# Kernel optimization log

Measured on AMD Instinct MI355X. Metric: run time of the kernel, lower is better.

## Reference

```python
import jax, jax.numpy as jnp
import numpy as np

N_NODES = 100000
N_EDGES = 3200000
IN_DIM = 256
OUT_DIM = 128


def setup_inputs() -> dict:
    key = jax.random.key(0)
    k1, k2, k3, k4, k5 = jax.random.split(key, 5)
    # node features
    x = jax.random.normal(k1, (N_NODES, IN_DIM), dtype=jnp.float32)
    # glorot-uniform weight as in glorot_init
    init_range = np.sqrt(6.0 / (IN_DIM + OUT_DIM)).astype(np.float32)
    weight = jax.random.uniform(k2, (IN_DIM, OUT_DIM), dtype=jnp.float32,
                                minval=-init_range, maxval=init_range)
    # sparse adjacency in COO form: adj[dst, src] = edge_weight
    edge_src = jax.random.randint(k3, (N_EDGES,), 0, N_NODES, dtype=jnp.int64)
    edge_dst = jax.random.randint(k4, (N_EDGES,), 0, N_NODES, dtype=jnp.int64)
    edge_weight = jax.random.uniform(k5, (N_EDGES,), dtype=jnp.float32)
    return {"x": x, "weight": weight, "edge_weight": edge_weight,
            "edge_src": edge_src, "edge_dst": edge_dst}


def reference(x, weight, edge_weight, edge_src, edge_dst):
    # dense feature transform: [N, in] @ [in, out] -> [N, out]
    xw = x @ weight
    # sparse adjacency matmul (adj @ xw) as gather + weighted scatter-add
    msgs = xw[edge_src] * edge_weight[:, None]           # [E, out]
    agg = jax.ops.segment_sum(msgs, edge_dst, num_segments=N_NODES)
    # fused activation
    return jax.nn.relu(agg)
```

## Files before the change

### kernel.cpp

```cpp
#include <hip/hip_runtime.h>

#define IN_DIM 256
#define OUT_DIM 128
#define BM 64
#define BKG 64

#define BSHIFT 7
#define BNODES 128
#define MAXB2 1024
#define CHUNK1 4096
#define CAPB 4736

typedef __attribute__((ext_vector_type(4))) float floatx4;
typedef __attribute__((ext_vector_type(8))) short shortx8;

static __device__ __forceinline__ unsigned short f2bf(float f) {
  unsigned u = __float_as_uint(f);
  u += 0x7FFFu + ((u >> 16) & 1u);
  return (unsigned short)(u >> 16);
}

struct GemmSmem {
  unsigned short As[BM][BKG + 8];
  unsigned short Bs[OUT_DIM][BKG + 8];
};
struct PartSmem {
  uint2 srec[CHUNK1];
  int hcnt[MAXB2];
  int loff[MAXB2];
  int lcur[MAXB2];
  int gbase[MAXB2];
  int sh[256];
};
#define SMEM3 ((sizeof(GemmSmem) > sizeof(PartSmem)) ? sizeof(GemmSmem) : sizeof(PartSmem))

__global__ __launch_bounds__(256) void prep_wt_kernel(
    const float* __restrict__ w, unsigned short* __restrict__ wt) {
  const int idx = blockIdx.x * 256 + threadIdx.x;
  const int k = idx >> 7;
  const int n = idx & 127;
  wt[n * IN_DIM + k] = f2bf(w[idx]);
}

static __device__ void do_gemm_block(int bid, const float* __restrict__ x,
                                     const unsigned short* __restrict__ wt,
                                     unsigned short* __restrict__ xw,
                                     int n_nodes, char* smem) {
  GemmSmem* sm = (GemmSmem*)smem;
  const int t = threadIdx.x;
  const int wv = t >> 6;
  const int lane = t & 63;
  const int quad = lane >> 4;
  const int l16 = lane & 15;
  const int row0 = bid * BM;
  if (row0 >= n_nodes) return;

  floatx4 acc[4][2];
#pragma unroll
  for (int a = 0; a < 4; ++a)
#pragma unroll
    for (int b = 0; b < 2; ++b) acc[a][b] = (floatx4){0.f, 0.f, 0.f, 0.f};

  for (int k0 = 0; k0 < IN_DIM; k0 += BKG) {
    __syncthreads();
#pragma unroll
    for (int i = 0; i < 4; ++i) {
      const int idx = i * 256 + t;
      const int r = idx >> 4;
      const int kq = (idx & 15) * 4;
      int row = row0 + r;
      if (row >= n_nodes) row = n_nodes - 1;
      const float4 v = *(const float4*)(x + (size_t)row * IN_DIM + k0 + kq);
      ushort4 sv;
      sv.x = f2bf(v.x); sv.y = f2bf(v.y); sv.z = f2bf(v.z); sv.w = f2bf(v.w);
      *(ushort4*)&sm->As[r][kq] = sv;
    }
#pragma unroll
    for (int i = 0; i < 4; ++i) {
      const int idx16 = i * 256 + t;
      const int n = idx16 >> 3;
      const int off = (idx16 & 7) * 8;
      *(int4*)&sm->Bs[n][off] =
          *(const int4*)(wt + (size_t)n * IN_DIM + k0 + off);
    }
    __syncthreads();

#pragma unroll
    for (int kk = 0; kk < BKG; kk += 32) {
      shortx8 af[4];
#pragma unroll
      for (int tm = 0; tm < 4; ++tm)
        af[tm] = *(const shortx8*)&sm->As[tm * 16 + l16][kk + quad * 8];
      shortx8 bfr[2];
#pragma unroll
      for (int tn = 0; tn < 2; ++tn)
        bfr[tn] =
            *(const shortx8*)&sm->Bs[wv * 32 + tn * 16 + l16][kk + quad * 8];
#pragma unroll
      for (int tm = 0; tm < 4; ++tm)
#pragma unroll
        for (int tn = 0; tn < 2; ++tn)
          acc[tm][tn] = __builtin_amdgcn_mfma_f32_16x16x32_bf16(
              af[tm], bfr[tn], acc[tm][tn], 0, 0, 0);
    }
  }

#pragma unroll
  for (int tm = 0; tm < 4; ++tm)
#pragma unroll
    for (int tn = 0; tn < 2; ++tn)
#pragma unroll
      for (int r = 0; r < 4; ++r) {
        const int grow = row0 + tm * 16 + quad * 4 + r;
        const int gcol = wv * 32 + tn * 16 + l16;
        if (grow < n_nodes)
          xw[(size_t)grow * OUT_DIM + gcol] = f2bf(acc[tm][tn][r]);
      }
}

static __device__ void do_partition_block(
    int bid, const int* __restrict__ esrc, const int* __restrict__ edst,
    const float* __restrict__ ew, int* __restrict__ btail,
    uint2* __restrict__ csr2, int n_edges, int nb2, char* smem) {
  PartSmem* sm = (PartSmem*)smem;
  const int t = threadIdx.x;
  const int base = bid * CHUNK1;
  const int cn = min(CHUNK1, n_edges - base);

  for (int b = t; b < MAXB2; b += 256) sm->hcnt[b] = 0;
  __syncthreads();

  int dst[16];
  unsigned xpk[16];
#pragma unroll
  for (int i = 0; i < 16; ++i) {
    const int idx = t + i * 256;
    if (idx < cn) {
      const int e = base + idx;
      dst[i] = edst[e];
      unsigned wb = __float_as_uint(ew[e]);
      wb += 0x7FFFu + ((wb >> 16) & 1u);
      xpk[i] = ((wb >> 16) << 17) | (unsigned)esrc[e];
      atomicAdd(&sm->hcnt[((unsigned)dst[i]) >> BSHIFT], 1);
    } else {
      dst[i] = -1;
    }
  }
  __syncthreads();
  {
    const int b4 = 4 * t;
    const int a0 = sm->hcnt[b4], a1 = sm->hcnt[b4 + 1];
    const int a2 = sm->hcnt[b4 + 2], a3 = sm->hcnt[b4 + 3];
    const int s = a0 + a1 + a2 + a3;
    sm->sh[t] = s;
    __syncthreads();
    for (int off = 1; off < 256; off <<= 1) {
      const int add = (t >= off) ? sm->sh[t - off] : 0;
      __syncthreads();
      sm->sh[t] += add;
      __syncthreads();
    }
    int run = sm->sh[t] - s;
    sm->loff[b4] = run; sm->lcur[b4] = run; run += a0;
    sm->loff[b4 + 1] = run; sm->lcur[b4 + 1] = run; run += a1;
    sm->loff[b4 + 2] = run; sm->lcur[b4 + 2] = run; run += a2;
    sm->loff[b4 + 3] = run; sm->lcur[b4 + 3] = run;
  }
  __syncthreads();
  for (int b = t; b < nb2; b += 256) {
    const int c = sm->hcnt[b];
    if (c) sm->gbase[b] = b * CAPB + atomicAdd(&btail[b], c);
  }
  __syncthreads();
#pragma unroll
  for (int i = 0; i < 16; ++i)
    if (dst[i] >= 0) {
      const int bk = ((unsigned)dst[i]) >> BSHIFT;
      const int p = atomicAdd(&sm->lcur[bk], 1);
      sm->srec[p] = make_uint2(xpk[i], (unsigned)dst[i]);
    }
  __syncthreads();
  for (int i = t; i < cn; i += 256) {
    const uint2 r = sm->srec[i];
    const int bk = r.y >> BSHIFT;
    const size_t pos = (size_t)sm->gbase[bk] + (i - sm->loff[bk]);
    if (pos < (size_t)(bk + 1) * CAPB) csr2[pos] = r;
  }
}

__global__ __launch_bounds__(256) void fused_part_gemm_kernel(
    const int* __restrict__ esrc, const int* __restrict__ edst,
    const float* __restrict__ ew, int* __restrict__ btail,
    uint2* __restrict__ csr2, int n_edges, int nb2, int pb,
    const float* __restrict__ x, const unsigned short* __restrict__ wt,
    unsigned short* __restrict__ xw, int n_nodes) {
  __shared__ __align__(16) char smem[SMEM3];
  if ((int)blockIdx.x < pb)
    do_partition_block(blockIdx.x, esrc, edst, ew, btail, csr2, n_edges, nb2,
                       smem);
  else
    do_gemm_block(blockIdx.x - pb, x, wt, xw, n_nodes, smem);
}

struct AggSmem {
  unsigned xin[CAPB];
  unsigned xs[CAPB];
  unsigned char db[CAPB];
  int ncnt[BNODES];
  int lcur[BNODES];
  int sst[BNODES];
  int sen[BNODES];
  int sh[256];
};

__global__ __launch_bounds__(256) void sort_agg_kernel(
    const uint2* __restrict__ csr2, const int* __restrict__ btail,
    const unsigned short* __restrict__ xw, float* __restrict__ out,
    int n_nodes) {
  __shared__ __align__(16) AggSmem sm;
  const int t = threadIdx.x;
  const int b = blockIdx.x;
  const int node0 = b << BSHIFT;
  const size_t S = (size_t)b * CAPB;
  const int cnt = min(btail[b], CAPB);

  for (int i = t; i < cnt; i += 256) {
    const uint2 r = csr2[S + i];
    sm.xin[i] = r.x;
    sm.db[i] = (unsigned char)(r.y & (BNODES - 1));
  }
  if (t < BNODES) sm.ncnt[t] = 0;
  __syncthreads();
  for (int i = t; i < cnt; i += 256) atomicAdd(&sm.ncnt[sm.db[i]], 1);
  __syncthreads();
  {
    const int s = (t < BNODES) ? sm.ncnt[t] : 0;
    sm.sh[t] = s;
    __syncthreads();
    for (int off = 1; off < 256; off <<= 1) {
      const int add = (t >= off) ? sm.sh[t - off] : 0;
      __syncthreads();
      sm.sh[t] += add;
      __syncthreads();
    }
    if (t < BNODES) {
      const int run = sm.sh[t] - s;
      sm.lcur[t] = run;
      sm.sst[t] = run;
      sm.sen[t] = run + s;
    }
  }
  __syncthreads();
  for (int i = t; i < cnt; i += 256) {
    const int p = atomicAdd(&sm.lcur[sm.db[i]], 1);
    sm.xs[p] = sm.xin[i];
  }
  __syncthreads();

  const int g = t >> 4;
  const int lane = t & 15;
  const int d8 = lane * 8;

  for (int nl = g; nl < BNODES; nl += 16) {
    const int node = node0 + nl;
    if (node >= n_nodes) continue;
    const int j0 = sm.sst[nl];
    const int j1 = sm.sen[nl];

    float a0 = 0.f, a1 = 0.f, a2 = 0.f, a3 = 0.f;
    float a4 = 0.f, a5 = 0.f, a6 = 0.f, a7 = 0.f;
    float c0 = 0.f, c1 = 0.f, c2 = 0.f, c3 = 0.f;
    float c4 = 0.f, c5 = 0.f, c6 = 0.f, c7 = 0.f;

    int j = j0;
    for (; j + 4 <= j1; j += 4) {
      const unsigned p0 = sm.xs[j];
      const unsigned p1 = sm.xs[j + 1];
      const unsigned p2 = sm.xs[j + 2];
      const unsigned p3 = sm.xs[j + 3];
      const uint4 v0 = *(const uint4*)(xw + (size_t)(p0 & 0x1FFFFu) * OUT_DIM + d8);
      const uint4 v1 = *(const uint4*)(xw + (size_t)(p1 & 0x1FFFFu) * OUT_DIM + d8);
      const uint4 v2 = *(const uint4*)(xw + (size_t)(p2 & 0x1FFFFu) * OUT_DIM + d8);
      const uint4 v3 = *(const uint4*)(xw + (size_t)(p3 & 0x1FFFFu) * OUT_DIM + d8);
      const float w0 = __uint_as_float((p0 >> 17) << 16);
      const float w1 = __uint_as_float((p1 >> 17) << 16);
      const float w2 = __uint_as_float((p2 >> 17) << 16);
      const float w3 = __uint_as_float((p3 >> 17) << 16);
      a0 = fmaf(__uint_as_float(v0.x << 16), w0, a0);
      a1 = fmaf(__uint_as_float(v0.x & 0xFFFF0000u), w0, a1);
      a2 = fmaf(__uint_as_float(v0.y << 16), w0, a2);
      a3 = fmaf(__uint_as_float(v0.y & 0xFFFF0000u), w0, a3);
      a4 = fmaf(__uint_as_float(v0.z << 16), w0, a4);
      a5 = fmaf(__uint_as_float(v0.z & 0xFFFF0000u), w0, a5);
      a6 = fmaf(__uint_as_float(v0.w << 16), w0, a6);
      a7 = fmaf(__uint_as_float(v0.w & 0xFFFF0000u), w0, a7);
      c0 = fmaf(__uint_as_float(v1.x << 16), w1, c0);
      c1 = fmaf(__uint_as_float(v1.x & 0xFFFF0000u), w1, c1);
      c2 = fmaf(__uint_as_float(v1.y << 16), w1, c2);
      c3 = fmaf(__uint_as_float(v1.y & 0xFFFF0000u), w1, c3);
      c4 = fmaf(__uint_as_float(v1.z << 16), w1, c4);
      c5 = fmaf(__uint_as_float(v1.z & 0xFFFF0000u), w1, c5);
      c6 = fmaf(__uint_as_float(v1.w << 16), w1, c6);
      c7 = fmaf(__uint_as_float(v1.w & 0xFFFF0000u), w1, c7);
      a0 = fmaf(__uint_as_float(v2.x << 16), w2, a0);
      a1 = fmaf(__uint_as_float(v2.x & 0xFFFF0000u), w2, a1);
      a2 = fmaf(__uint_as_float(v2.y << 16), w2, a2);
      a3 = fmaf(__uint_as_float(v2.y & 0xFFFF0000u), w2, a3);
      a4 = fmaf(__uint_as_float(v2.z << 16), w2, a4);
      a5 = fmaf(__uint_as_float(v2.z & 0xFFFF0000u), w2, a5);
      a6 = fmaf(__uint_as_float(v2.w << 16), w2, a6);
      a7 = fmaf(__uint_as_float(v2.w & 0xFFFF0000u), w2, a7);
      c0 = fmaf(__uint_as_float(v3.x << 16), w3, c0);
      c1 = fmaf(__uint_as_float(v3.x & 0xFFFF0000u), w3, c1);
      c2 = fmaf(__uint_as_float(v3.y << 16), w3, c2);
      c3 = fmaf(__uint_as_float(v3.y & 0xFFFF0000u), w3, c3);
      c4 = fmaf(__uint_as_float(v3.z << 16), w3, c4);
      c5 = fmaf(__uint_as_float(v3.z & 0xFFFF0000u), w3, c5);
      c6 = fmaf(__uint_as_float(v3.w << 16), w3, c6);
      c7 = fmaf(__uint_as_float(v3.w & 0xFFFF0000u), w3, c7);
    }
    for (; j < j1; ++j) {
      const unsigned p0 = sm.xs[j];
      const float w0 = __uint_as_float((p0 >> 17) << 16);
      const uint4 v0 = *(const uint4*)(xw + (size_t)(p0 & 0x1FFFFu) * OUT_DIM + d8);
      a0 = fmaf(__uint_as_float(v0.x << 16), w0, a0);
      a1 = fmaf(__uint_as_float(v0.x & 0xFFFF0000u), w0, a1);
      a2 = fmaf(__uint_as_float(v0.y << 16), w0, a2);
      a3 = fmaf(__uint_as_float(v0.y & 0xFFFF0000u), w0, a3);
      a4 = fmaf(__uint_as_float(v0.z << 16), w0, a4);
      a5 = fmaf(__uint_as_float(v0.z & 0xFFFF0000u), w0, a5);
      a6 = fmaf(__uint_as_float(v0.w << 16), w0, a6);
      a7 = fmaf(__uint_as_float(v0.w & 0xFFFF0000u), w0, a7);
    }

    float4 o0, o1;
    o0.x = fmaxf(a0 + c0, 0.f); o0.y = fmaxf(a1 + c1, 0.f);
    o0.z = fmaxf(a2 + c2, 0.f); o0.w = fmaxf(a3 + c3, 0.f);
    o1.x = fmaxf(a4 + c4, 0.f); o1.y = fmaxf(a5 + c5, 0.f);
    o1.z = fmaxf(a6 + c6, 0.f); o1.w = fmaxf(a7 + c7, 0.f);
    float* orow = out + (size_t)node * OUT_DIM + d8;
    *(float4*)orow = o0;
    *(float4*)(orow + 4) = o1;
  }
}

extern "C" void kernel_launch(void* const* d_in, const int* in_sizes, int n_in,
                              void* d_out, int out_size, void* d_ws,
                              size_t ws_size, hipStream_t stream) {
  const float* x    = (const float*)d_in[0];
  const float* w    = (const float*)d_in[1];
  const float* ew   = (const float*)d_in[2];
  const int*   esrc = (const int*)d_in[3];
  const int*   edst = (const int*)d_in[4];
  float* out = (float*)d_out;

  const int n_edges = in_sizes[2];
  const int n_nodes = out_size / OUT_DIM;
  const int nb2 = (n_nodes + BNODES - 1) >> BSHIFT;

  char* p = (char*)d_ws;
  unsigned short* xw = (unsigned short*)p;
  p += (size_t)n_nodes * OUT_DIM * sizeof(unsigned short);
  p = (char*)(((uintptr_t)p + 15) & ~(uintptr_t)15);
  unsigned short* wt = (unsigned short*)p;
  p += (size_t)OUT_DIM * IN_DIM * sizeof(unsigned short);
  p = (char*)(((uintptr_t)p + 15) & ~(uintptr_t)15);
  uint2* csr2 = (uint2*)p;  p += (size_t)nb2 * CAPB * sizeof(uint2);
  int* btail = (int*)p;     p += (size_t)nb2 * sizeof(int);

  hipMemsetAsync(btail, 0, (size_t)nb2 * sizeof(int), stream);

  prep_wt_kernel<<<(IN_DIM * OUT_DIM) / 256, 256, 0, stream>>>(w, wt);

  const int pblocks = (n_edges + CHUNK1 - 1) / CHUNK1;
  const int ngemm = (n_nodes + BM - 1) / BM;
  fused_part_gemm_kernel<<<pblocks + ngemm, 256, 0, stream>>>(
      esrc, edst, ew, btail, csr2, n_edges, nb2, pblocks, x, wt, xw, n_nodes);

  sort_agg_kernel<<<nb2, 256, 0, stream>>>(csr2, btail, xw, out, n_nodes);
}
```

Before: 387.8 us.

## Split fused partition/GEMM kernel, enlarge GEMM tile, stream csr reads in aggregation

Breaks the fused partition+GEMM launch into two separate kernels, so each one uses only its own shared memory footprint instead of the max of both. The GEMM row tile grows from 64 to 128 rows per block, which reuses the weight tile across more rows. The sort-aggregate kernel drops its xin/db shared staging and reads csr2 from global memory twice, which lowers LDS use and may raise occupancy. The cost is losing concurrent overlap of partition and GEMM blocks, plus an extra global read pass over csr2.

```diff
diff --git a/kernel.cpp b/kernel.cpp
--- a/kernel.cpp
+++ b/kernel.cpp
@@ -2,7 +2,7 @@
 
 #define IN_DIM 256
 #define OUT_DIM 128
-#define BM 64
+#define BM 128
 #define BKG 64
 
 #define BSHIFT 7
@@ -19,20 +19,6 @@
   u += 0x7FFFu + ((u >> 16) & 1u);
   return (unsigned short)(u >> 16);
 }
-
-struct GemmSmem {
-  unsigned short As[BM][BKG + 8];
-  unsigned short Bs[OUT_DIM][BKG + 8];
-};
-struct PartSmem {
-  uint2 srec[CHUNK1];
-  int hcnt[MAXB2];
-  int loff[MAXB2];
-  int lcur[MAXB2];
-  int gbase[MAXB2];
-  int sh[256];
-};
-#define SMEM3 ((sizeof(GemmSmem) > sizeof(PartSmem)) ? sizeof(GemmSmem) : sizeof(PartSmem))
 
 __global__ __launch_bounds__(256) void prep_wt_kernel(
     const float* __restrict__ w, unsigned short* __restrict__ wt) {
@@ -42,29 +28,30 @@
   wt[n * IN_DIM + k] = f2bf(w[idx]);
 }
 
-static __device__ void do_gemm_block(int bid, const float* __restrict__ x,
-                                     const unsigned short* __restrict__ wt,
-                                     unsigned short* __restrict__ xw,
-                                     int n_nodes, char* smem) {
-  GemmSmem* sm = (GemmSmem*)smem;
+__global__ __launch_bounds__(256) void gemm_xw_kernel(
+    const float* __restrict__ x, const unsigned short* __restrict__ wt,
+    unsigned short* __restrict__ xw, int n_nodes) {
+  __shared__ unsigned short As[BM][BKG + 8];
+  __shared__ unsigned short Bs[OUT_DIM][BKG + 8];
+
   const int t = threadIdx.x;
   const int wv = t >> 6;
   const int lane = t & 63;
   const int quad = lane >> 4;
   const int l16 = lane & 15;
-  const int row0 = bid * BM;
+  const int row0 = blockIdx.x * BM;
   if (row0 >= n_nodes) return;
 
-  floatx4 acc[4][2];
-#pragma unroll
-  for (int a = 0; a < 4; ++a)
+  floatx4 acc[8][2];
+#pragma unroll
+  for (int a = 0; a < 8; ++a)
 #pragma unroll
     for (int b = 0; b < 2; ++b) acc[a][b] = (floatx4){0.f, 0.f, 0.f, 0.f};
 
   for (int k0 = 0; k0 < IN_DIM; k0 += BKG) {
     __syncthreads();
 #pragma unroll
-    for (int i = 0; i < 4; ++i) {
+    for (int i = 0; i < 8; ++i) {
       const int idx = i * 256 + t;
       const int r = idx >> 4;
       const int kq = (idx & 15) * 4;
@@ -73,40 +60,36 @@
       const float4 v = *(const float4*)(x + (size_t)row * IN_DIM + k0 + kq);
       ushort4 sv;
       sv.x = f2bf(v.x); sv.y = f2bf(v.y); sv.z = f2bf(v.z); sv.w = f2bf(v.w);
-      *(ushort4*)&sm->As[r][kq] = sv;
+      *(ushort4*)&As[r][kq] = sv;
     }
 #pragma unroll
     for (int i = 0; i < 4; ++i) {
       const int idx16 = i * 256 + t;
       const int n = idx16 >> 3;
       const int off = (idx16 & 7) * 8;
-      *(int4*)&sm->Bs[n][off] =
-          *(const int4*)(wt + (size_t)n * IN_DIM + k0 + off);
+      *(int4*)&Bs[n][off] = *(const int4*)(wt + (size_t)n * IN_DIM + k0 + off);
     }
     __syncthreads();
 
 #pragma unroll
     for (int kk = 0; kk < BKG; kk += 32) {
-      shortx8 af[4];
-#pragma unroll
-      for (int tm = 0; tm < 4; ++tm)
-        af[tm] = *(const shortx8*)&sm->As[tm * 16 + l16][kk + quad * 8];
       shortx8 bfr[2];
 #pragma unroll
       for (int tn = 0; tn < 2; ++tn)
-        bfr[tn] =
-            *(const shortx8*)&sm->Bs[wv * 32 + tn * 16 + l16][kk + quad * 8];
-#pragma unroll
-      for (int tm = 0; tm < 4; ++tm)
-#pragma unroll
-        for (int tn = 0; tn < 2; ++tn)
-          acc[tm][tn] = __builtin_amdgcn_mfma_f32_16x16x32_bf16(
-              af[tm], bfr[tn], acc[tm][tn], 0, 0, 0);
-    }
-  }
-
-#pragma unroll
-  for (int tm = 0; tm < 4; ++tm)
+        bfr[tn] = *(const shortx8*)&Bs[wv * 32 + tn * 16 + l16][kk + quad * 8];
+#pragma unroll
+      for (int tm = 0; tm < 8; ++tm) {
+        const shortx8 af = *(const shortx8*)&As[tm * 16 + l16][kk + quad * 8];
+        acc[tm][0] = __builtin_amdgcn_mfma_f32_16x16x32_bf16(af, bfr[0],
+                                                             acc[tm][0], 0, 0, 0);
+        acc[tm][1] = __builtin_amdgcn_mfma_f32_16x16x32_bf16(af, bfr[1],
+                                                             acc[tm][1], 0, 0, 0);
+      }
+    }
+  }
+
+#pragma unroll
+  for (int tm = 0; tm < 8; ++tm)
 #pragma unroll
     for (int tn = 0; tn < 2; ++tn)
 #pragma unroll
@@ -118,16 +101,21 @@
       }
 }
 
-static __device__ void do_partition_block(
-    int bid, const int* __restrict__ esrc, const int* __restrict__ edst,
+__global__ __launch_bounds__(256) void partition_kernel(
+    const int* __restrict__ esrc, const int* __restrict__ edst,
     const float* __restrict__ ew, int* __restrict__ btail,
-    uint2* __restrict__ csr2, int n_edges, int nb2, char* smem) {
-  PartSmem* sm = (PartSmem*)smem;
+    uint2* __restrict__ csr2, int n_edges, int nb2) {
+  __shared__ uint2 srec[CHUNK1];
+  __shared__ int hcnt[MAXB2];
+  __shared__ int loff[MAXB2];
+  __shared__ int lcur[MAXB2];
+  __shared__ int gbase[MAXB2];
+  __shared__ int sh[256];
   const int t = threadIdx.x;
-  const int base = bid * CHUNK1;
+  const int base = blockIdx.x * CHUNK1;
   const int cn = min(CHUNK1, n_edges - base);
 
-  for (int b = t; b < MAXB2; b += 256) sm->hcnt[b] = 0;
+  for (int b = t; b < MAXB2; b += 256) hcnt[b] = 0;
   __syncthreads();
 
   int dst[16];
@@ -141,7 +129,7 @@
       unsigned wb = __float_as_uint(ew[e]);
       wb += 0x7FFFu + ((wb >> 16) & 1u);
       xpk[i] = ((wb >> 16) << 17) | (unsigned)esrc[e];
-      atomicAdd(&sm->hcnt[((unsigned)dst[i]) >> BSHIFT], 1);
+      atomicAdd(&hcnt[((unsigned)dst[i]) >> BSHIFT], 1);
     } else {
       dst[i] = -1;
     }
@@ -149,63 +137,47 @@
   __syncthreads();
   {
     const int b4 = 4 * t;
-    const int a0 = sm->hcnt[b4], a1 = sm->hcnt[b4 + 1];
-    const int a2 = sm->hcnt[b4 + 2], a3 = sm->hcnt[b4 + 3];
+    const int a0 = hcnt[b4], a1 = hcnt[b4 + 1];
+    const int a2 = hcnt[b4 + 2], a3 = hcnt[b4 + 3];
     const int s = a0 + a1 + a2 + a3;
-    sm->sh[t] = s;
+    sh[t] = s;
     __syncthreads();
     for (int off = 1; off < 256; off <<= 1) {
-      const int add = (t >= off) ? sm->sh[t - off] : 0;
+      const int add = (t >= off) ? sh[t - off] : 0;
       __syncthreads();
-      sm->sh[t] += add;
+      sh[t] += add;
       __syncthreads();
     }
-    int run = sm->sh[t] - s;
-    sm->loff[b4] = run; sm->lcur[b4] = run; run += a0;
-    sm->loff[b4 + 1] = run; sm->lcur[b4 + 1] = run; run += a1;
-    sm->loff[b4 + 2] = run; sm->lcur[b4 + 2] = run; run += a2;
-    sm->loff[b4 + 3] = run; sm->lcur[b4 + 3] = run;
+    int run = sh[t] - s;
+    loff[b4] = run; lcur[b4] = run; run += a0;
+    loff[b4 + 1] = run; lcur[b4 + 1] = run; run += a1;
+    loff[b4 + 2] = run; lcur[b4 + 2] = run; run += a2;
+    loff[b4 + 3] = run; lcur[b4 + 3] = run;
   }
   __syncthreads();
   for (int b = t; b < nb2; b += 256) {
-    const int c = sm->hcnt[b];
-    if (c) sm->gbase[b] = b * CAPB + atomicAdd(&btail[b], c);
+    const int c = hcnt[b];
+    if (c) gbase[b] = b * CAPB + atomicAdd(&btail[b], c);
   }
   __syncthreads();
 #pragma unroll
   for (int i = 0; i < 16; ++i)
     if (dst[i] >= 0) {
       const int bk = ((unsigned)dst[i]) >> BSHIFT;
-      const int p = atomicAdd(&sm->lcur[bk], 1);
-      sm->srec[p] = make_uint2(xpk[i], (unsigned)dst[i]);
+      const int p = atomicAdd(&lcur[bk], 1);
+      srec[p] = make_uint2(xpk[i], (unsigned)dst[i]);
     }
   __syncthreads();
   for (int i = t; i < cn; i += 256) {
-    const uint2 r = sm->srec[i];
+    const uint2 r = srec[i];
     const int bk = r.y >> BSHIFT;
-    const size_t pos = (size_t)sm->gbase[bk] + (i - sm->loff[bk]);
+    const size_t pos = (size_t)gbase[bk] + (i - loff[bk]);
     if (pos < (size_t)(bk + 1) * CAPB) csr2[pos] = r;
   }
 }
 
-__global__ __launch_bounds__(256) void fused_part_gemm_kernel(
-    const int* __restrict__ esrc, const int* __restrict__ edst,
-    const float* __restrict__ ew, int* __restrict__ btail,
-    uint2* __restrict__ csr2, int n_edges, int nb2, int pb,
-    const float* __restrict__ x, const unsigned short* __restrict__ wt,
-    unsigned short* __restrict__ xw, int n_nodes) {
-  __shared__ __align__(16) char smem[SMEM3];
-  if ((int)blockIdx.x < pb)
-    do_partition_block(blockIdx.x, esrc, edst, ew, btail, csr2, n_edges, nb2,
-                       smem);
-  else
-    do_gemm_block(blockIdx.x - pb, x, wt, xw, n_nodes, smem);
-}
-
 struct AggSmem {
-  unsigned xin[CAPB];
   unsigned xs[CAPB];
-  unsigned char db[CAPB];
   int ncnt[BNODES];
   int lcur[BNODES];
   int sst[BNODES];
@@ -224,14 +196,10 @@
   const size_t S = (size_t)b * CAPB;
   const int cnt = min(btail[b], CAPB);
 
-  for (int i = t; i < cnt; i += 256) {
-    const uint2 r = csr2[S + i];
-    sm.xin[i] = r.x;
-    sm.db[i] = (unsigned char)(r.y & (BNODES - 1));
-  }
   if (t < BNODES) sm.ncnt[t] = 0;
   __syncthreads();
-  for (int i = t; i < cnt; i += 256) atomicAdd(&sm.ncnt[sm.db[i]], 1);
+  for (int i = t; i < cnt; i += 256)
+    atomicAdd(&sm.ncnt[csr2[S + i].y & (BNODES - 1)], 1);
   __syncthreads();
   {
     const int s = (t < BNODES) ? sm.ncnt[t] : 0;
@@ -252,8 +220,9 @@
   }
   __syncthreads();
   for (int i = t; i < cnt; i += 256) {
-    const int p = atomicAdd(&sm.lcur[sm.db[i]], 1);
-    sm.xs[p] = sm.xin[i];
+    const uint2 r = csr2[S + i];
+    const int p = atomicAdd(&sm.lcur[r.y & (BNODES - 1)], 1);
+    sm.xs[p] = r.x;
   }
   __syncthreads();
 
@@ -373,9 +342,11 @@
   prep_wt_kernel<<<(IN_DIM * OUT_DIM) / 256, 256, 0, stream>>>(w, wt);
 
   const int pblocks = (n_edges + CHUNK1 - 1) / CHUNK1;
-  const int ngemm = (n_nodes + BM - 1) / BM;
-  fused_part_gemm_kernel<<<pblocks + ngemm, 256, 0, stream>>>(
-      esrc, edst, ew, btail, csr2, n_edges, nb2, pblocks, x, wt, xw, n_nodes);
+  partition_kernel<<<pblocks, 256, 0, stream>>>(esrc, edst, ew, btail, csr2,
+                                                n_edges, nb2);
+
+  gemm_xw_kernel<<<(n_nodes + BM - 1) / BM, 256, 0, stream>>>(x, wt, xw,
+                                                              n_nodes);
 
   sort_agg_kernel<<<nb2, 256, 0, stream>>>(csr2, btail, xw, out, n_nodes);
 }
```

Result: no change. 395.3 us (+1.9%).
